# Kernel tuning notes

Hardware: AMD Instinct MI355X
Metric: run time of the kernel (lower is better)

## Reference

```python
import jax, jax.numpy as jnp
import numpy as np

V, D, NL, K = 50257, 768, 12, 4095  # vocab, d_model, n_layers, l_max (odd => SAME conv)
B, L = 2, 4095


def _longconv(x, w, b):
    """Depthwise long cross-correlation via FFT.
    x: (B, L, D), w: (D, K), b: (D,). SAME padding p=K//2 (K odd -> out len L).
    y[t,d] = sum_k w[d,k] * x[t+k-p, d]  (zeros outside), matching torch Conv1d.
    """
    Bn, Ln, Dn = x.shape
    Kn = w.shape[1]
    p = Kn // 2
    n = Ln + 2 * p
    nfft = 1 << int(np.ceil(np.log2(n + Kn - 1)))
    xp = jnp.pad(x, ((0, 0), (p, p), (0, 0)))          # (B, n, D)
    wf = jnp.flip(w, axis=1).T                          # (K, D) time-reversed kernel
    X = jnp.fft.rfft(xp, n=nfft, axis=1)                # (B, F, D)
    Wf = jnp.fft.rfft(wf, n=nfft, axis=0)               # (F, D)
    y = jnp.fft.irfft(X * Wf[None], n=nfft, axis=1)     # linear conv
    # cross-correlation output t = full-conv index t + K - 1
    return y[:, Kn - 1:Kn - 1 + Ln, :] + b


def _layernorm(x, g, b, eps=1e-5):
    m = jnp.mean(x, axis=-1, keepdims=True)
    v = jnp.var(x, axis=-1, keepdims=True)
    return (x - m) * jax.lax.rsqrt(v + eps) * g + b


def setup_inputs() -> dict:
    key = jax.random.key(0)
    ks = jax.random.split(key, 8)
    input_ids = jax.random.randint(ks[0], (B, L), 0, V)
    emb = jax.random.normal(ks[1], (V, D), dtype=jnp.float32) * 0.02
    pos_emb = jax.random.normal(ks[2], (4095, D), dtype=jnp.float32) * 0.02
    # small filter scale so 12 residual long-conv layers stay numerically tame
    filt_w = jax.random.normal(ks[3], (NL, D, K), dtype=jnp.float32) * (0.1 / np.sqrt(K))
    filt_b = jax.random.normal(ks[4], (NL, D), dtype=jnp.float32) * 0.01
    ln_g = jnp.ones((D,), dtype=jnp.float32)
    ln_b = jnp.zeros((D,), dtype=jnp.float32)
    qa_w = jax.random.normal(ks[5], (D, 2), dtype=jnp.float32) * 0.02
    qa_b = jnp.zeros((2,), dtype=jnp.float32)
    return {"input_ids": input_ids, "emb": emb, "pos_emb": pos_emb,
            "filt_w": filt_w, "filt_b": filt_b, "ln_g": ln_g, "ln_b": ln_b,
            "qa_w": qa_w, "qa_b": qa_b}


def reference(input_ids, emb, pos_emb, filt_w, filt_b, ln_g, ln_b, qa_w, qa_b):
    Ln = input_ids.shape[1]
    x = emb[input_ids] + pos_emb[jnp.arange(Ln)][None]   # (B, L, D)
    for i in range(filt_w.shape[0]):                     # 12 stacked Hyena layers
        x = x + _longconv(x, filt_w[i], filt_b[i])
    x = _layernorm(x, ln_g, ln_b)
    logits = x @ qa_w + qa_b                             # (B, L, 2)
    return logits[..., 0], logits[..., 1]
```

## Files before the change

kernel.cpp:

```cpp
#include <hip/hip_runtime.h>


#define LSEQ   4095
#define DMODEL 768
#define KF     4095
#define CROW   4096
#define NCH    1536
#define BL     8190

typedef _Float16 f16x8 __attribute__((ext_vector_type(8)));
typedef _Float16 f16x4 __attribute__((ext_vector_type(4)));
typedef float    f32x4 __attribute__((ext_vector_type(4)));

__global__ __launch_bounds__(256)
void embed_kernel(const int* __restrict__ ids, const float* __restrict__ emb,
                  const float* __restrict__ pos, float* __restrict__ xout)
{
    __shared__ float tile[32 * 65];
    const int d0 = blockIdx.x * 64;
    const int t0 = blockIdx.y * 32;
    const int b  = blockIdx.z;
    const int tid = threadIdx.x;

    {
        const int lane = tid & 63, row = tid >> 6;
        #pragma unroll
        for (int r = 0; r < 8; ++r) {
            int tr = row * 8 + r;
            int t  = t0 + tr;
            if (t < LSEQ) {
                int id = ids[b * LSEQ + t];
                tile[tr * 65 + lane] =
                    emb[(size_t)id * DMODEL + d0 + lane] +
                    pos[(size_t)t  * DMODEL + d0 + lane];
            }
        }
    }
    __syncthreads();
    {
        const int lt = tid & 31, drow = tid >> 5;
        #pragma unroll
        for (int r = 0; r < 8; ++r) {
            int dr = drow * 8 + r;
            int t  = t0 + lt;
            if (t < LSEQ)
                xout[(size_t)(b * DMODEL + d0 + dr) * CROW + t] = tile[lt * 65 + dr];
        }
    }
}

__global__ __launch_bounds__(256, 2)
void conv_kernel(const float* __restrict__ xin, float* __restrict__ xout,
                 const float* __restrict__ w, const float* __restrict__ bias)
{
    __shared__ __align__(16) _Float16 lxh[8704];
    __shared__ __align__(16) _Float16 wsh[2 * 2112];

    const int c    = blockIdx.x;
    const int du   = __builtin_amdgcn_readfirstlane(c % DMODEL);
    const int tid  = threadIdx.x;
    const size_t choff = (size_t)c * CROW;
    const float* __restrict__ wrow = w + (size_t)du * KF;
    const float* __restrict__ xrow = xin + choff;
    const float bv = bias[du];

    const int lane = tid & 63;
    const int wid  = tid >> 6;
    const int jj   = lane & 15;
    const int hh   = lane >> 4;
    const int T0   = wid << 2;

    const int abase = 256 * T0 + 16 * jj + 8 * hh;
    const int bbase = 264 * (jj & 7) + 8 * (hh - (jj >> 3) + 1);

    auto wbuild = [&](int bufi, int bb) {
        for (int cc = tid; cc < 264; cc += 256) {
            int r  = cc / 33;
            int q  = cc - 33 * r;
            int wb = 256 * bb - 9 + 8 * q - r;
            f16x8 hw;
            if (bb >= 1 && bb <= 14) {
                float4 va = *(const float4*)(wrow + wb);
                float4 vb = *(const float4*)(wrow + wb + 4);
                hw[0] = (_Float16)va.x; hw[1] = (_Float16)va.y;
                hw[2] = (_Float16)va.z; hw[3] = (_Float16)va.w;
                hw[4] = (_Float16)vb.x; hw[5] = (_Float16)vb.y;
                hw[6] = (_Float16)vb.z; hw[7] = (_Float16)vb.w;
            } else {
                #pragma unroll
                for (int e = 0; e < 8; ++e) {
                    int wi = wb + e;
                    hw[e] = (_Float16)(((unsigned)wi < 4095u) ? wrow[wi] : 0.0f);
                }
            }
            *(f16x8*)(wsh + bufi * 2112 + 264 * r + 8 * q) = hw;
        }
    };

    {
        f16x8 z = {};
        *(f16x8*)(lxh + 8 * tid) = z;
        *(f16x8*)(lxh + 8 * (768 + tid)) = z;
        if (tid < 64) *(f16x8*)(lxh + 8 * (1024 + tid)) = z;
        #pragma unroll
        for (int rr = 0; rr < 4; ++rr) {
            float4 a = ((const float4*)xrow)[tid + 256 * rr];
            f16x4 hv;
            hv[0] = (_Float16)a.x; hv[1] = (_Float16)a.y;
            hv[2] = (_Float16)a.z; hv[3] = (_Float16)a.w;
            *(f16x4*)(lxh + 2048 + 4 * (tid + 256 * rr)) = hv;
        }
    }
    wbuild(0, 0);
    __syncthreads();

    f32x4 acc[4];
    {
        f32x4 z4 = {};
        #pragma unroll
        for (int m = 0; m < 4; ++m) acc[m] = z4;
    }

    f16x8 ring[32];
    #pragma unroll
    for (int u = 0; u < 32; ++u)
        ring[u] = *(const f16x8*)(lxh + abase + 32 * u);

#define BLOCK8(PH, BETA)                                                      \
    {                                                                         \
      wbuild(((PH) ^ 1) & 1, (BETA) + 1);                                     \
      _Pragma("unroll")                                                       \
      for (int d = 0; d < 8; ++d) {                                           \
        f16x8 bf = *(const f16x8*)(wsh + ((PH) & 1) * 2112 + bbase + 32 * d); \
        acc[0] = __builtin_amdgcn_mfma_f32_16x16x32_f16(                      \
                     ring[(8 * (PH) + d) & 31], bf, acc[0], 0, 0, 0);         \
        acc[1] = __builtin_amdgcn_mfma_f32_16x16x32_f16(                      \
                     ring[(8 * (PH) + d + 8) & 31], bf, acc[1], 0, 0, 0);     \
        acc[2] = __builtin_amdgcn_mfma_f32_16x16x32_f16(                      \
                     ring[(8 * (PH) + d + 16) & 31], bf, acc[2], 0, 0, 0);    \
        acc[3] = __builtin_amdgcn_mfma_f32_16x16x32_f16(                      \
                     ring[(8 * (PH) + d + 24) & 31], bf, acc[3], 0, 0, 0);    \
        ring[(8 * (PH) + d) & 31] =                                           \
            *(const f16x8*)(lxh + abase + 32 * (8 * (BETA) + d + 32));        \
      }                                                                       \
      __syncthreads();                                                        \
    }

    int beta = 0;
    #pragma unroll 1
    for (int s4 = 0; s4 < 4; ++s4) {
        BLOCK8(0, beta) ++beta;
        BLOCK8(1, beta) ++beta;
        BLOCK8(2, beta) ++beta;
        BLOCK8(3, beta) ++beta;
    }
    BLOCK8(0, 16)
#undef BLOCK8

    #pragma unroll
    for (int m = 0; m < 4; ++m) {
        int T = T0 + m;
        #pragma unroll
        for (int p = 0; p < 4; ++p) {
            int t = 256 * T + 64 * hh + 16 * p + jj;
            float v = acc[m][p] + bv + xrow[t];
            xout[choff + t] = (t < LSEQ) ? v : 0.0f;
        }
    }
}

__global__ __launch_bounds__(256)
void head_kernel(const float* __restrict__ x, const float* __restrict__ g,
                 const float* __restrict__ bb, const float* __restrict__ qw,
                 const float* __restrict__ qb, float* __restrict__ out)
{
    const int b = blockIdx.y;
    const int t = blockIdx.x * 256 + threadIdx.x;
    const bool valid = t < LSEQ;
    const int tt = valid ? t : 0;

    float s1 = 0.f, s2 = 0.f, q0 = 0.f, q1 = 0.f;
    float G0 = 0.f, G1 = 0.f, C0 = 0.f, C1 = 0.f;
    const float* xb = x + (size_t)b * DMODEL * CROW + tt;
    for (int dd = 0; dd < DMODEL; ++dd) {
        float xv = xb[(size_t)dd * CROW];
        float gd = g[dd], bd = bb[dd];
        float w0 = qw[2 * dd], w1 = qw[2 * dd + 1];
        s1 += xv;
        s2 = fmaf(xv, xv, s2);
        q0 = fmaf(xv, gd * w0, q0);
        q1 = fmaf(xv, gd * w1, q1);
        G0 = fmaf(gd, w0, G0); G1 = fmaf(gd, w1, G1);
        C0 = fmaf(bd, w0, C0); C1 = fmaf(bd, w1, C1);
    }
    float m   = s1 * (1.0f / 768.0f);
    float var = s2 * (1.0f / 768.0f) - m * m;
    float r   = rsqrtf(var + 1e-5f);
    float l0  = r * (q0 - m * G0) + C0 + qb[0];
    float l1  = r * (q1 - m * G1) + C1 + qb[1];
    if (valid) {
        out[(size_t)b * LSEQ + t] = l0;
        out[BL + (size_t)b * LSEQ + t] = l1;
    }
}

extern "C" void kernel_launch(void* const* d_in, const int* in_sizes, int n_in,
                              void* d_out, int out_size, void* d_ws, size_t ws_size,
                              hipStream_t stream)
{
    const int*   ids = (const int*)  d_in[0];
    const float* emb = (const float*)d_in[1];
    const float* pos = (const float*)d_in[2];
    const float* fw  = (const float*)d_in[3];
    const float* fb  = (const float*)d_in[4];
    const float* lg  = (const float*)d_in[5];
    const float* lb  = (const float*)d_in[6];
    const float* qw  = (const float*)d_in[7];
    const float* qb  = (const float*)d_in[8];
    float* out = (float*)d_out;

    const size_t bufElems = (size_t)NCH * CROW;
    if (ws_size < 2 * bufElems * sizeof(float)) return;

    float* bufA = (float*)d_ws;
    float* bufB = bufA + bufElems;
    hipMemsetAsync(bufA, 0, bufElems * sizeof(float), stream);

    embed_kernel<<<dim3(12, 128, 2), 256, 0, stream>>>(ids, emb, pos, bufA);

    const float* cur = bufA;
    float*       nxt = bufB;
    for (int l = 0; l < 12; ++l) {
        conv_kernel<<<NCH, 256, 0, stream>>>(cur, nxt,
                                             fw + (size_t)l * DMODEL * KF,
                                             fb + (size_t)l * DMODEL);
        const float* tmp = nxt;
        nxt = (float*)cur;
        cur = tmp;
    }
    head_kernel<<<dim3(16, 2), 256, 0, stream>>>(cur, lg, lb, qw, qb, out);
}
```

Measured before the change: 1.063 ms.

## Software-pipeline filter weight loads across MFMA block and drop workspace memset

Global loads of the next filter block are issued before the MFMA loop, and their conversion and LDS stores happen after it, so load latency overlaps the matrix math. LDS B-fragments are preloaded into registers, s_setprio raises wave priority during the MFMA section, and the last block skips the unneeded build. The embed kernel now writes zeros in the padding column, so the full-buffer memset is removed. This raises register pressure, which could hurt occupancy at launch_bounds(256,2).

```diff
diff --git a/kernel.cpp b/kernel.cpp
--- a/kernel.cpp
+++ b/kernel.cpp
@@ -43,8 +43,8 @@
         for (int r = 0; r < 8; ++r) {
             int dr = drow * 8 + r;
             int t  = t0 + lt;
-            if (t < LSEQ)
-                xout[(size_t)(b * DMODEL + d0 + dr) * CROW + t] = tile[lt * 65 + dr];
+            float v = (t < LSEQ) ? tile[lt * 65 + dr] : 0.0f;
+            xout[(size_t)(b * DMODEL + d0 + dr) * CROW + t] = v;
         }
     }
 }
@@ -73,25 +73,23 @@
     const int abase = 256 * T0 + 16 * jj + 8 * hh;
     const int bbase = 264 * (jj & 7) + 8 * (hh - (jj >> 3) + 1);
 
-    auto wbuild = [&](int bufi, int bb) {
+    const int r0 = tid / 33, q0 = tid - 33 * r0;
+    const int dsoff0 = 264 * r0 + 8 * q0;
+    const int wboff0 = 8 * q0 - r0 - 9;
+    const int q1 = tid + 256 - 231;
+    const int dsoff1 = 264 * 7 + 8 * q1;
+    const int wboff1 = 8 * q1 - 7 - 9;
+
+    auto wbuild_full = [&](int bufi, int bb) {
         for (int cc = tid; cc < 264; cc += 256) {
             int r  = cc / 33;
             int q  = cc - 33 * r;
             int wb = 256 * bb - 9 + 8 * q - r;
             f16x8 hw;
-            if (bb >= 1 && bb <= 14) {
-                float4 va = *(const float4*)(wrow + wb);
-                float4 vb = *(const float4*)(wrow + wb + 4);
-                hw[0] = (_Float16)va.x; hw[1] = (_Float16)va.y;
-                hw[2] = (_Float16)va.z; hw[3] = (_Float16)va.w;
-                hw[4] = (_Float16)vb.x; hw[5] = (_Float16)vb.y;
-                hw[6] = (_Float16)vb.z; hw[7] = (_Float16)vb.w;
-            } else {
-                #pragma unroll
-                for (int e = 0; e < 8; ++e) {
-                    int wi = wb + e;
-                    hw[e] = (_Float16)(((unsigned)wi < 4095u) ? wrow[wi] : 0.0f);
-                }
+            #pragma unroll
+            for (int e = 0; e < 8; ++e) {
+                int wi = wb + e;
+                hw[e] = (_Float16)(((unsigned)wi < 4095u) ? wrow[wi] : 0.0f);
             }
             *(f16x8*)(wsh + bufi * 2112 + 264 * r + 8 * q) = hw;
         }
@@ -111,7 +109,7 @@
             *(f16x4*)(lxh + 2048 + 4 * (tid + 256 * rr)) = hv;
         }
     }
-    wbuild(0, 0);
+    wbuild_full(0, 0);
     __syncthreads();
 
     f32x4 acc[4];
@@ -126,35 +124,83 @@
     for (int u = 0; u < 32; ++u)
         ring[u] = *(const f16x8*)(lxh + abase + 32 * u);
 
-#define BLOCK8(PH, BETA)                                                      \
+#define BLOCK8(PH, BETA, DO_BUILD)                                            \
     {                                                                         \
-      wbuild(((PH) ^ 1) & 1, (BETA) + 1);                                     \
+      float wv0[8]; float wv1[8];                                             \
+      if (DO_BUILD) {                        \
+        const int bb  = (BETA) + 1;                                           \
+        const int wb0 = wboff0 + 256 * bb;                                    \
+        if (bb <= 14) {                        \
+          float4 va = *(const float4*)(wrow + wb0);                           \
+          float4 vb = *(const float4*)(wrow + wb0 + 4);                       \
+          wv0[0] = va.x; wv0[1] = va.y; wv0[2] = va.z; wv0[3] = va.w;         \
+          wv0[4] = vb.x; wv0[5] = vb.y; wv0[6] = vb.z; wv0[7] = vb.w;         \
+          if (tid < 8) {                                                      \
+            const int wb1 = wboff1 + 256 * bb;                                \
+            float4 vc = *(const float4*)(wrow + wb1);                         \
+            float4 vd = *(const float4*)(wrow + wb1 + 4);                     \
+            wv1[0] = vc.x; wv1[1] = vc.y; wv1[2] = vc.z; wv1[3] = vc.w;       \
+            wv1[4] = vd.x; wv1[5] = vd.y; wv1[6] = vd.z; wv1[7] = vd.w;       \
+          }                                                                   \
+        } else {                                   \
+          _Pragma("unroll")                                                   \
+          for (int e = 0; e < 8; ++e) {                                       \
+            int wi = wb0 + e;                                                 \
+            wv0[e] = ((unsigned)wi < 4095u) ? wrow[wi] : 0.0f;                \
+          }                                                                   \
+          if (tid < 8) {                                                      \
+            const int wb1 = wboff1 + 256 * bb;                                \
+            _Pragma("unroll")                                                 \
+            for (int e = 0; e < 8; ++e) {                                     \
+              int wi = wb1 + e;                                               \
+              wv1[e] = ((unsigned)wi < 4095u) ? wrow[wi] : 0.0f;              \
+            }                                                                 \
+          }                                                                   \
+        }                                                                     \
+      }                                                                       \
+      f16x8 bfv[8];                             \
+      _Pragma("unroll")                                                       \
+      for (int d = 0; d < 8; ++d)                                             \
+        bfv[d] = *(const f16x8*)(wsh + ((PH) & 1) * 2112 + bbase + 32 * d);   \
+      __builtin_amdgcn_s_setprio(1);                                         \
       _Pragma("unroll")                                                       \
       for (int d = 0; d < 8; ++d) {                                           \
-        f16x8 bf = *(const f16x8*)(wsh + ((PH) & 1) * 2112 + bbase + 32 * d); \
         acc[0] = __builtin_amdgcn_mfma_f32_16x16x32_f16(                      \
-                     ring[(8 * (PH) + d) & 31], bf, acc[0], 0, 0, 0);         \
+                     ring[(8 * (PH) + d) & 31], bfv[d], acc[0], 0, 0, 0);     \
         acc[1] = __builtin_amdgcn_mfma_f32_16x16x32_f16(                      \
-                     ring[(8 * (PH) + d + 8) & 31], bf, acc[1], 0, 0, 0);     \
+                     ring[(8 * (PH) + d + 8) & 31], bfv[d], acc[1], 0, 0, 0); \
         acc[2] = __builtin_amdgcn_mfma_f32_16x16x32_f16(                      \
-                     ring[(8 * (PH) + d + 16) & 31], bf, acc[2], 0, 0, 0);    \
+                     ring[(8 * (PH) + d + 16) & 31], bfv[d], acc[2], 0, 0, 0);\
         acc[3] = __builtin_amdgcn_mfma_f32_16x16x32_f16(                      \
-                     ring[(8 * (PH) + d + 24) & 31], bf, acc[3], 0, 0, 0);    \
+                     ring[(8 * (PH) + d + 24) & 31], bfv[d], acc[3], 0, 0, 0);\
         ring[(8 * (PH) + d) & 31] =                                           \
             *(const f16x8*)(lxh + abase + 32 * (8 * (BETA) + d + 32));        \
       }                                                                       \
+      __builtin_amdgcn_s_setprio(0);                                         \
+      if (DO_BUILD) {                              \
+        f16x8 hw0;                                                            \
+        _Pragma("unroll")                                                     \
+        for (int e = 0; e < 8; ++e) hw0[e] = (_Float16)wv0[e];                \
+        *(f16x8*)(wsh + (((PH) ^ 1) & 1) * 2112 + dsoff0) = hw0;              \
+        if (tid < 8) {                                                        \
+          f16x8 hw1;                                                          \
+          _Pragma("unroll")                                                   \
+          for (int e = 0; e < 8; ++e) hw1[e] = (_Float16)wv1[e];              \
+          *(f16x8*)(wsh + (((PH) ^ 1) & 1) * 2112 + dsoff1) = hw1;            \
+        }                                                                     \
+      }                                                                       \
       __syncthreads();                                                        \
     }
 
     int beta = 0;
     #pragma unroll 1
     for (int s4 = 0; s4 < 4; ++s4) {
-        BLOCK8(0, beta) ++beta;
-        BLOCK8(1, beta) ++beta;
-        BLOCK8(2, beta) ++beta;
-        BLOCK8(3, beta) ++beta;
-    }
-    BLOCK8(0, 16)
+        BLOCK8(0, beta, 1) ++beta;
+        BLOCK8(1, beta, 1) ++beta;
+        BLOCK8(2, beta, 1) ++beta;
+        BLOCK8(3, beta, 1) ++beta;
+    }
+    BLOCK8(0, 16, 0)
 #undef BLOCK8
 
     #pragma unroll
@@ -224,7 +270,6 @@
 
     float* bufA = (float*)d_ws;
     float* bufB = bufA + bufElems;
-    hipMemsetAsync(bufA, 0, bufElems * sizeof(float), stream);
 
     embed_kernel<<<dim3(12, 128, 2), 256, 0, stream>>>(ids, emb, pos, bufA);
 
```

Measured after the change: 1.098 ms. 1.03x slower.

## Give each wave a private weight buffer to drop per-block barriers in conv

Applied to the files above, without the earlier changes.

Each wave now builds its own double-buffered fp16 copy of the filter tile in LDS, which removes the __syncthreads after every 8-step block. Weight-build offsets are precomputed per lane, B fragments are loaded up front, and the MFMA section runs under raised wave priority. The embed kernel now writes zeros to the padding columns, so the full-buffer memset is dropped. The cost is four times the weight LDS and redundant global weight loads across waves, which may reduce occupancy. Correctness relies on each wave only reading the weights it wrote itself.

```diff
diff --git a/kernel.cpp b/kernel.cpp
--- a/kernel.cpp
+++ b/kernel.cpp
@@ -43,8 +43,8 @@
         for (int r = 0; r < 8; ++r) {
             int dr = drow * 8 + r;
             int t  = t0 + lt;
-            if (t < LSEQ)
-                xout[(size_t)(b * DMODEL + d0 + dr) * CROW + t] = tile[lt * 65 + dr];
+            float v = (t < LSEQ) ? tile[lt * 65 + dr] : 0.0f;
+            xout[(size_t)(b * DMODEL + d0 + dr) * CROW + t] = v;
         }
     }
 }
@@ -54,7 +54,7 @@
                  const float* __restrict__ w, const float* __restrict__ bias)
 {
     __shared__ __align__(16) _Float16 lxh[8704];
-    __shared__ __align__(16) _Float16 wsh[2 * 2112];
+    __shared__ __align__(16) _Float16 wsh[4 * 2 * 2112];
 
     const int c    = blockIdx.x;
     const int du   = __builtin_amdgcn_readfirstlane(c % DMODEL);
@@ -71,29 +71,66 @@
     const int T0   = wid << 2;
 
     const int abase = 256 * T0 + 16 * jj + 8 * hh;
+    _Float16* const wshw = wsh + wid * 4224;
     const int bbase = 264 * (jj & 7) + 8 * (hh - (jj >> 3) + 1);
 
+    int dsoff_k[5], wboff_k[5];
+    #pragma unroll
+    for (int k = 0; k < 5; ++k) {
+        int cc = lane + 64 * k;
+        int r  = cc / 33, q = cc - 33 * r;
+        dsoff_k[k] = 264 * r + 8 * q;
+        wboff_k[k] = 8 * q - r - 9;
+    }
+
     auto wbuild = [&](int bufi, int bb) {
-        for (int cc = tid; cc < 264; cc += 256) {
-            int r  = cc / 33;
-            int q  = cc - 33 * r;
-            int wb = 256 * bb - 9 + 8 * q - r;
-            f16x8 hw;
-            if (bb >= 1 && bb <= 14) {
-                float4 va = *(const float4*)(wrow + wb);
-                float4 vb = *(const float4*)(wrow + wb + 4);
+        _Float16* const dst = wshw + bufi * 2112;
+        if (bb >= 1 && bb <= 14) {
+            #pragma unroll
+            for (int k = 0; k < 4; ++k) {
+                const float* p = wrow + (wboff_k[k] + 256 * bb);
+                float4 va = *(const float4*)p;
+                float4 vb = *(const float4*)(p + 4);
+                f16x8 hw;
                 hw[0] = (_Float16)va.x; hw[1] = (_Float16)va.y;
                 hw[2] = (_Float16)va.z; hw[3] = (_Float16)va.w;
                 hw[4] = (_Float16)vb.x; hw[5] = (_Float16)vb.y;
                 hw[6] = (_Float16)vb.z; hw[7] = (_Float16)vb.w;
-            } else {
+                *(f16x8*)(dst + dsoff_k[k]) = hw;
+            }
+            if (lane < 8) {
+                const float* p = wrow + (wboff_k[4] + 256 * bb);
+                float4 va = *(const float4*)p;
+                float4 vb = *(const float4*)(p + 4);
+                f16x8 hw;
+                hw[0] = (_Float16)va.x; hw[1] = (_Float16)va.y;
+                hw[2] = (_Float16)va.z; hw[3] = (_Float16)va.w;
+                hw[4] = (_Float16)vb.x; hw[5] = (_Float16)vb.y;
+                hw[6] = (_Float16)vb.z; hw[7] = (_Float16)vb.w;
+                *(f16x8*)(dst + dsoff_k[4]) = hw;
+            }
+        } else {
+            #pragma unroll
+            for (int k = 0; k < 4; ++k) {
+                int wb = wboff_k[k] + 256 * bb;
+                f16x8 hw;
                 #pragma unroll
                 for (int e = 0; e < 8; ++e) {
                     int wi = wb + e;
                     hw[e] = (_Float16)(((unsigned)wi < 4095u) ? wrow[wi] : 0.0f);
                 }
-            }
-            *(f16x8*)(wsh + bufi * 2112 + 264 * r + 8 * q) = hw;
+                *(f16x8*)(dst + dsoff_k[k]) = hw;
+            }
+            if (lane < 8) {
+                int wb = wboff_k[4] + 256 * bb;
+                f16x8 hw;
+                #pragma unroll
+                for (int e = 0; e < 8; ++e) {
+                    int wi = wb + e;
+                    hw[e] = (_Float16)(((unsigned)wi < 4095u) ? wrow[wi] : 0.0f);
+                }
+                *(f16x8*)(dst + dsoff_k[4]) = hw;
+            }
         }
     };
 
@@ -126,35 +163,39 @@
     for (int u = 0; u < 32; ++u)
         ring[u] = *(const f16x8*)(lxh + abase + 32 * u);
 
-#define BLOCK8(PH, BETA)                                                      \
+#define BLOCK8(PH, BETA, DO_BUILD)                                            \
     {                                                                         \
-      wbuild(((PH) ^ 1) & 1, (BETA) + 1);                                     \
+      if (DO_BUILD) wbuild(((PH) ^ 1) & 1, (BETA) + 1);                       \
+      f16x8 bfv[8];                                                           \
+      _Pragma("unroll")                                                       \
+      for (int d = 0; d < 8; ++d)                                             \
+        bfv[d] = *(const f16x8*)(wshw + ((PH) & 1) * 2112 + bbase + 32 * d);  \
+      __builtin_amdgcn_s_setprio(1);                                         \
       _Pragma("unroll")                                                       \
       for (int d = 0; d < 8; ++d) {                                           \
-        f16x8 bf = *(const f16x8*)(wsh + ((PH) & 1) * 2112 + bbase + 32 * d); \
         acc[0] = __builtin_amdgcn_mfma_f32_16x16x32_f16(                      \
-                     ring[(8 * (PH) + d) & 31], bf, acc[0], 0, 0, 0);         \
+                     ring[(8 * (PH) + d) & 31], bfv[d], acc[0], 0, 0, 0);     \
         acc[1] = __builtin_amdgcn_mfma_f32_16x16x32_f16(                      \
-                     ring[(8 * (PH) + d + 8) & 31], bf, acc[1], 0, 0, 0);     \
+                     ring[(8 * (PH) + d + 8) & 31], bfv[d], acc[1], 0, 0, 0); \
         acc[2] = __builtin_amdgcn_mfma_f32_16x16x32_f16(                      \
-                     ring[(8 * (PH) + d + 16) & 31], bf, acc[2], 0, 0, 0);    \
+                     ring[(8 * (PH) + d + 16) & 31], bfv[d], acc[2], 0, 0, 0);\
         acc[3] = __builtin_amdgcn_mfma_f32_16x16x32_f16(                      \
-                     ring[(8 * (PH) + d + 24) & 31], bf, acc[3], 0, 0, 0);    \
+                     ring[(8 * (PH) + d + 24) & 31], bfv[d], acc[3], 0, 0, 0);\
         ring[(8 * (PH) + d) & 31] =                                           \
             *(const f16x8*)(lxh + abase + 32 * (8 * (BETA) + d + 32));        \
       }                                                                       \
-      __syncthreads();                                                        \
+      __builtin_amdgcn_s_setprio(0);                                         \
     }
 
     int beta = 0;
     #pragma unroll 1
     for (int s4 = 0; s4 < 4; ++s4) {
-        BLOCK8(0, beta) ++beta;
-        BLOCK8(1, beta) ++beta;
-        BLOCK8(2, beta) ++beta;
-        BLOCK8(3, beta) ++beta;
-    }
-    BLOCK8(0, 16)
+        BLOCK8(0, beta, 1) ++beta;
+        BLOCK8(1, beta, 1) ++beta;
+        BLOCK8(2, beta, 1) ++beta;
+        BLOCK8(3, beta, 1) ++beta;
+    }
+    BLOCK8(0, 16, 0)
 #undef BLOCK8
 
     #pragma unroll
@@ -224,7 +265,6 @@
 
     float* bufA = (float*)d_ws;
     float* bufB = bufA + bufElems;
-    hipMemsetAsync(bufA, 0, bufElems * sizeof(float), stream);
 
     embed_kernel<<<dim3(12, 128, 2), 256, 0, stream>>>(ids, emb, pos, bufA);
 
```

New measurement: 1.688 ms. +58.8%, slower.
